# Kernel tuning notes

Measured on AMD Instinct MI355X. Metric: run time of the kernel, lower is better.

Reference implementation:

```python
import jax, jax.numpy as jnp
import numpy as np

N_EMBED = 1024
N_HEADS = 16
HEAD_SIZE = N_EMBED // N_HEADS
B, T = 4, 2048
LN_EPS = 1e-5


def _layer_norm(x, gamma, beta):
    mu = jnp.mean(x, axis=-1, keepdims=True)
    var = jnp.var(x, axis=-1, keepdims=True)
    return (x - mu) * jax.lax.rsqrt(var + LN_EPS) * gamma + beta


def setup_inputs() -> dict:
    key = jax.random.key(0)
    ks = jax.random.split(key, 12)
    s = 1.0 / np.sqrt(N_EMBED)
    sh = 1.0 / np.sqrt(4 * N_EMBED)
    return {
        "x": jax.random.normal(ks[0], (B, T, N_EMBED), jnp.float32),
        "Wk": jax.random.uniform(ks[1], (N_EMBED, N_EMBED), jnp.float32, -s, s),
        "Wq": jax.random.uniform(ks[2], (N_EMBED, N_EMBED), jnp.float32, -s, s),
        "Wv": jax.random.uniform(ks[3], (N_EMBED, N_EMBED), jnp.float32, -s, s),
        "Wproj": jax.random.uniform(ks[4], (N_EMBED, N_EMBED), jnp.float32, -s, s),
        "bproj": jax.random.uniform(ks[5], (N_EMBED,), jnp.float32, -s, s),
        "W1": jax.random.uniform(ks[6], (N_EMBED, 4 * N_EMBED), jnp.float32, -s, s),
        "b1": jax.random.uniform(ks[7], (4 * N_EMBED,), jnp.float32, -s, s),
        "W2": jax.random.uniform(ks[8], (4 * N_EMBED, N_EMBED), jnp.float32, -sh, sh),
        "b2": jax.random.uniform(ks[9], (N_EMBED,), jnp.float32, -sh, sh),
        "g1": jnp.ones((N_EMBED,), jnp.float32),
        "beta1": jnp.zeros((N_EMBED,), jnp.float32),
        "g2": jnp.ones((N_EMBED,), jnp.float32),
        "beta2": jnp.zeros((N_EMBED,), jnp.float32),
    }


def reference(x, Wk, Wq, Wv, Wproj, bproj, W1, b1, W2, b2, g1, beta1, g2, beta2):
    Bt, Tt, C = x.shape
    h = _layer_norm(x, g1, beta1)
    # project and split heads: (B, H, T, D)
    def heads(W):
        return (h @ W).reshape(Bt, Tt, N_HEADS, HEAD_SIZE).transpose(0, 2, 1, 3)
    q, k, v = heads(Wq), heads(Wk), heads(Wv)
    wei = jnp.einsum("bhtd,bhsd->bhts", q, k) / np.sqrt(HEAD_SIZE)
    causal = jnp.tril(jnp.ones((Tt, Tt), bool))
    wei = jnp.where(causal, wei, -jnp.inf)
    wei = jax.nn.softmax(wei, axis=-1)
    out = jnp.einsum("bhts,bhsd->bhtd", wei, v)
    out = out.transpose(0, 2, 1, 3).reshape(Bt, Tt, C)
    x = x + out @ Wproj + bproj
    h2 = _layer_norm(x, g2, beta2)
    ff = jax.nn.relu(h2 @ W1 + b1) @ W2 + b2
    return x + ff
```

## Files before the change

kernel.cpp:

```cpp
#include <hip/hip_runtime.h>
#include <stdint.h>

typedef __bf16 bf16x8 __attribute__((ext_vector_type(8)));
typedef float f32x4 __attribute__((ext_vector_type(4)));
typedef unsigned short u16x8 __attribute__((ext_vector_type(8)));
typedef unsigned short u16x4 __attribute__((ext_vector_type(4)));
typedef unsigned int u32x2 __attribute__((ext_vector_type(2)));
typedef float fvec4 __attribute__((ext_vector_type(4)));

__device__ __forceinline__ unsigned short f2b(float f) {
  unsigned u = __builtin_bit_cast(unsigned, f);
  return (unsigned short)((u + 0x7fffu + ((u >> 16) & 1u)) >> 16);
}

__device__ __forceinline__ bf16x8 ldfrag(const unsigned short* p) {
  return __builtin_bit_cast(bf16x8, *(const u16x8*)p);
}

__device__ __forceinline__ float fexp2(float x) {
  float r;
  asm("v_exp_f32 %0, %1" : "=v"(r) : "v"(x));
  return r;
}

__device__ __forceinline__ unsigned cvtpk(float a, float b) {
  unsigned r;
  asm("v_cvt_pk_bf16_f32 %0, %1, %2" : "=v"(r) : "v"(a), "v"(b));
  return r;
}

__device__ __forceinline__ void gload_lds16(const void* g, void* l) {
  auto gp = reinterpret_cast<const __attribute__((address_space(1))) void*>(
      reinterpret_cast<uintptr_t>(g));
  auto lp = reinterpret_cast<__attribute__((address_space(3))) void*>(
      reinterpret_cast<uintptr_t>(l));
  __builtin_amdgcn_global_load_lds(gp, lp, 16, 0, 0);
}

__global__ void transpose_cast(const float* __restrict__ W, unsigned short* __restrict__ Wt,
                               int K, int N) {
  __shared__ float tile[32][33];
  const int n0 = blockIdx.x * 32, k0 = blockIdx.y * 32;
  const int tx = threadIdx.x, ty = threadIdx.y;
#pragma unroll
  for (int j = 0; j < 4; ++j)
    tile[ty + j * 8][tx] = W[(size_t)(k0 + ty + j * 8) * N + n0 + tx];
  __syncthreads();
#pragma unroll
  for (int j = 0; j < 4; ++j)
    Wt[(size_t)(n0 + ty + j * 8) * K + k0 + tx] = f2b(tile[tx][ty + j * 8]);
}

__global__ void ln_kernel(const float* __restrict__ X, const float* __restrict__ g,
                          const float* __restrict__ be, unsigned short* __restrict__ H) {
  const int row = (blockIdx.x * blockDim.x + threadIdx.x) >> 6;
  const int l = threadIdx.x & 63;
  const float* xr = X + (size_t)row * 1024;
  fvec4 v[4];
  float s = 0.f, sq = 0.f;
#pragma unroll
  for (int i = 0; i < 4; ++i) {
    v[i] = *(const fvec4*)(xr + i * 256 + l * 4);
#pragma unroll
    for (int j = 0; j < 4; ++j) { s += v[i][j]; sq += v[i][j] * v[i][j]; }
  }
#pragma unroll
  for (int off = 32; off >= 1; off >>= 1) {
    s += __shfl_xor(s, off);
    sq += __shfl_xor(sq, off);
  }
  const float mean = s * (1.f / 1024.f);
  const float var = sq * (1.f / 1024.f) - mean * mean;
  const float rstd = rsqrtf(var + 1e-5f);
#pragma unroll
  for (int i = 0; i < 4; ++i) {
    const int col = i * 256 + l * 4;
    fvec4 gg = *(const fvec4*)(g + col);
    fvec4 bb = *(const fvec4*)(be + col);
    u16x4 o;
#pragma unroll
    for (int j = 0; j < 4; ++j) o[j] = f2b((v[i][j] - mean) * rstd * gg[j] + bb[j]);
    *(u16x4*)(H + (size_t)row * 1024 + col) = o;
  }
}

template <int BM, int BN, int WM, int WN, int NBUF, int NTH, int EPI>
__global__ __launch_bounds__(NTH, 2) void gemm8p(
    const unsigned short* __restrict__ A, const unsigned short* __restrict__ Bt,
    const float* __restrict__ bias, const float* __restrict__ resid,
    float* __restrict__ Cf, unsigned short* __restrict__ Cb,
    unsigned short* __restrict__ pK, unsigned short* __restrict__ pVT,
    int M, int N, int K, int ntiles) {
  constexpr int BK = 32;
  constexpr int ASZ = BM * BK * 2;
  constexpr int BSZ = BN * BK * 2;
  constexpr int BUFSZ = ASZ + BSZ;
  constexpr int NW = NTH / 64;
  static_assert(WM * WN == NW, "wave grid");
  constexpr int MF = BM / (WM * 16);
  constexpr int NF = BN / (WN * 16);
  constexpr int UA = ASZ / (NTH * 16);
  constexpr int UB = BSZ / (NTH * 16);
  constexpr int UNITS = UA + UB;
  constexpr int VMSTEADY = (NBUF - 2) * UNITS;
  static_assert(UA * NTH * 16 == ASZ && UB * NTH * 16 == BSZ, "unit split");
  __shared__ __align__(16) char lds[NBUF * BUFSZ];

  const int tid = threadIdx.x;
  const int w = tid >> 6, l = tid & 63;
  const int wr = w / WN, wc = w % WN;
  const int kg = l >> 4, fr = l & 15;
  const int xtiles = N / BN;
  const int nblk = (int)gridDim.x;

  int Aoff[MF], Boff[NF];
#pragma unroll
  for (int m = 0; m < MF; ++m) {
    const int r = wr * (MF * 16) + m * 16 + fr;
    Aoff[m] = r * 64 + ((kg * 16) ^ (((r >> 1) & 3) << 4));
  }
#pragma unroll
  for (int n = 0; n < NF; ++n) {
    const int r = wc * (NF * 16) + n * 16 + fr;
    Boff[n] = ASZ + r * 64 + ((kg * 16) ^ (((r >> 1) & 3) << 4));
  }

  for (int tl = (int)blockIdx.x; tl < ntiles; tl += nblk) {
    if (tl != (int)blockIdx.x) __builtin_amdgcn_s_barrier();
    const int q8 = ntiles >> 3;
    const int swz = (tl & 7) * q8 + (tl >> 3);
    const size_t am0 = (size_t)(swz / xtiles) * BM;
    const size_t bn0 = (size_t)(swz % xtiles) * BN;

    const char* src[UNITS];
#pragma unroll
    for (int u = 0; u < UA; ++u) {
      const int flatq = u * NTH + tid;
      const int row = flatq >> 2;
      const int scb = ((flatq & 3) << 4) ^ (((row >> 1) & 3) << 4);
      src[u] = (const char*)(A + (am0 + row) * K) + scb;
    }
#pragma unroll
    for (int u = 0; u < UB; ++u) {
      const int flatq = u * NTH + tid;
      const int row = flatq >> 2;
      const int scb = ((flatq & 3) << 4) ^ (((row >> 1) & 3) << 4);
      src[UA + u] = (const char*)(Bt + (bn0 + row) * K) + scb;
    }

    f32x4 acc[MF][NF];
#pragma unroll
    for (int m = 0; m < MF; ++m)
#pragma unroll
      for (int n = 0; n < NF; ++n) acc[m][n] = (f32x4){0.f, 0.f, 0.f, 0.f};

    auto stage = [&](int sb) {
#pragma unroll
      for (int u = 0; u < UNITS; ++u) {
        gload_lds16(src[u], lds + sb * BUFSZ + u * (NTH * 16) + tid * 16);
        src[u] += 64;
      }
    };

    const int NT = K / BK;
#pragma unroll
    for (int p = 0; p < NBUF - 1; ++p) stage(p);
    asm volatile("s_waitcnt vmcnt(%0)" ::"i"(VMSTEADY) : "memory");
    __builtin_amdgcn_s_barrier();

    int cb0 = 0, sb = NBUF - 1;
    for (int kt = 0; kt < NT; ++kt) {
      if (kt + NBUF - 1 < NT) stage(sb);
      bf16x8 af[MF], bf[NF];
#pragma unroll
      for (int m = 0; m < MF; ++m)
        af[m] = ldfrag((const unsigned short*)(lds + cb0 + Aoff[m]));
#pragma unroll
      for (int n = 0; n < NF; ++n)
        bf[n] = ldfrag((const unsigned short*)(lds + cb0 + Boff[n]));
      __builtin_amdgcn_s_setprio(1);
#pragma unroll
      for (int m = 0; m < MF; ++m)
#pragma unroll
        for (int n = 0; n < NF; ++n)
          acc[m][n] = __builtin_amdgcn_mfma_f32_16x16x32_bf16(af[m], bf[n], acc[m][n], 0, 0, 0);
      __builtin_amdgcn_s_setprio(0);
      if (kt + NBUF - 1 < NT) {
        asm volatile("s_waitcnt vmcnt(%0)" ::"i"(VMSTEADY) : "memory");
        __builtin_amdgcn_s_barrier();
      } else if (kt + 2 < NT) {
        asm volatile("s_waitcnt vmcnt(%0)" ::"i"(UNITS) : "memory");
        __builtin_amdgcn_s_barrier();
      } else if (kt + 1 < NT) {
        asm volatile("s_waitcnt vmcnt(0)" ::: "memory");
        __builtin_amdgcn_s_barrier();
      }
      cb0 += BUFSZ;
      if (cb0 == NBUF * BUFSZ) cb0 = 0;
      sb += 1;
      if (sb == NBUF) sb = 0;
    }

#pragma unroll
    for (int m = 0; m < MF; ++m) {
      const size_t row0 = am0 + wr * (MF * 16) + m * 16 + kg * 4;
#pragma unroll
      for (int n = 0; n < NF; ++n) {
        const size_t col = bn0 + wc * (NF * 16) + n * 16 + fr;
        if (EPI == 3) {
          if (bn0 < 1024) {
#pragma unroll
            for (int r = 0; r < 4; ++r) Cb[(row0 + r) * 1024 + col] = f2b(acc[m][n][r]);
          } else if (bn0 < 2048) {
#pragma unroll
            for (int r = 0; r < 4; ++r) pK[(row0 + r) * 1024 + col - 1024] = f2b(acc[m][n][r]);
          } else {
            const int c2 = (int)col - 2048;
            const int hh = c2 >> 6, dd = c2 & 63;
            const int bb = (int)(row0 >> 11), tt = (int)(row0 & 2047);
            u16x4 pv;
#pragma unroll
            for (int r = 0; r < 4; ++r) pv[r] = f2b(acc[m][n][r]);
            *(u16x4*)(pVT + (((size_t)bb * 16 + hh) * 64 + dd) * 2048 + tt) = pv;
          }
        } else {
          const float bv = (EPI >= 1) ? bias[col] : 0.f;
#pragma unroll
          for (int r = 0; r < 4; ++r) {
            const size_t idx = (row0 + r) * N + col;
            float v = acc[m][n][r] + bv;
            if (EPI == 1) v = fmaxf(v, 0.f);
            if (EPI == 2) {
              Cf[idx] = v + resid[idx];
            } else {
              Cb[idx] = f2b(v);
            }
          }
        }
      }
    }
  }
}

#define PSTR 40
#define SC2 0.18033688f
__global__ __launch_bounds__(256, 3) void attn_kernel(const unsigned short* __restrict__ Qb,
                                                      const unsigned short* __restrict__ Kb,
                                                      const unsigned short* __restrict__ VT,
                                                      unsigned short* __restrict__ ATT) {
  __shared__ unsigned short Pl[4][32 * PSTR];
  const int tid = threadIdx.x;
  const int w = tid >> 6, l = tid & 63;
  const int kg = l >> 4, fr = l & 15;
  const int bh = blockIdx.x;
  const int b = bh >> 4, h = bh & 15;
  const int qt = 15 - (int)blockIdx.y;
  const int q0 = qt * 128 + w * 32;
  const size_t rbase = (size_t)b * 2048;
  const unsigned short* vtb = VT + (size_t)bh * 64 * 2048;

  bf16x8 bq[2][2];
#pragma unroll
  for (int qg = 0; qg < 2; ++qg) {
    const unsigned short* qrow = Qb + (rbase + q0 + qg * 16 + fr) * 1024 + h * 64;
#pragma unroll
    for (int c = 0; c < 2; ++c) bq[qg][c] = ldfrag(qrow + c * 32 + kg * 8);
  }

  f32x4 o[2][4];
#pragma unroll
  for (int qg = 0; qg < 2; ++qg)
#pragma unroll
    for (int nd = 0; nd < 4; ++nd) o[qg][nd] = (f32x4){0.f, 0.f, 0.f, 0.f};
  float m_run2[2] = {-1e30f, -1e30f}, l_run[2] = {0.f, 0.f};

  auto loadK = [&](int s0, bf16x8 (&ka)[2][2]) {
#pragma unroll
    for (int sg = 0; sg < 2; ++sg) {
      const unsigned short* krow = Kb + (rbase + s0 + sg * 16 + fr) * 1024 + h * 64;
      ka[sg][0] = ldfrag(krow + kg * 8);
      ka[sg][1] = ldfrag(krow + 32 + kg * 8);
    }
  };

  auto process = [&](int s0, bf16x8 (&ka)[2][2]) {
    bf16x8 vb[4];
#pragma unroll
    for (int nd = 0; nd < 4; ++nd)
      vb[nd] = ldfrag(vtb + (size_t)(nd * 16 + fr) * 2048 + s0 + kg * 8);

    f32x4 st[2][2];
#pragma unroll
    for (int sg = 0; sg < 2; ++sg)
#pragma unroll
      for (int qg = 0; qg < 2; ++qg) {
        st[sg][qg] = (f32x4){0.f, 0.f, 0.f, 0.f};
        st[sg][qg] = __builtin_amdgcn_mfma_f32_16x16x32_bf16(ka[sg][0], bq[qg][0], st[sg][qg], 0, 0, 0);
        st[sg][qg] = __builtin_amdgcn_mfma_f32_16x16x32_bf16(ka[sg][1], bq[qg][1], st[sg][qg], 0, 0, 0);
      }

#pragma unroll
    for (int qg = 0; qg < 2; ++qg) {
      const int qa = q0 + qg * 16 + fr;
      float vals[8];
      float tmax = -1e30f;
#pragma unroll
      for (int sg = 0; sg < 2; ++sg)
#pragma unroll
        for (int r = 0; r < 4; ++r) {
          const int sa = s0 + sg * 16 + kg * 4 + r;
          float v = (sa > qa) ? -1e30f : st[sg][qg][r];
          vals[sg * 4 + r] = v;
          tmax = fmaxf(tmax, v);
        }
      tmax = fmaxf(tmax, __shfl_xor(tmax, 16));
      tmax = fmaxf(tmax, __shfl_xor(tmax, 32));
      const float tm2 = tmax * SC2;
      if (__any(tm2 > m_run2[qg] + 8.f)) {
        const float m_new2 = fmaxf(m_run2[qg], tm2);
        const float alpha = fexp2(m_run2[qg] - m_new2);
        m_run2[qg] = m_new2;
        l_run[qg] *= alpha;
        float al[4];
#pragma unroll
        for (int r = 0; r < 4; ++r) al[r] = __shfl(alpha, kg * 4 + r);
#pragma unroll
        for (int nd = 0; nd < 4; ++nd)
#pragma unroll
          for (int r = 0; r < 4; ++r) o[qg][nd][r] *= al[r];
      }
      const float nm2 = -m_run2[qg];
      float psum = 0.f;
      unsigned pk[4];
#pragma unroll
      for (int i = 0; i < 4; ++i) {
        const float p0 = fexp2(__builtin_fmaf(vals[2 * i], SC2, nm2));
        const float p1 = fexp2(__builtin_fmaf(vals[2 * i + 1], SC2, nm2));
        psum += p0 + p1;
        pk[i] = cvtpk(p0, p1);
      }
      psum += __shfl_xor(psum, 16);
      psum += __shfl_xor(psum, 32);
      l_run[qg] += psum;
      u32x2 w0 = {pk[0], pk[1]};
      u32x2 w1 = {pk[2], pk[3]};
      *(u32x2*)(&Pl[w][(qg * 16 + fr) * PSTR + kg * 4]) = w0;
      *(u32x2*)(&Pl[w][(qg * 16 + fr) * PSTR + 16 + kg * 4]) = w1;
    }

    bf16x8 pa[2];
#pragma unroll
    for (int qg = 0; qg < 2; ++qg)
      pa[qg] = ldfrag(&Pl[w][(qg * 16 + fr) * PSTR + kg * 8]);
#pragma unroll
    for (int nd = 0; nd < 4; ++nd)
#pragma unroll
      for (int qg = 0; qg < 2; ++qg)
        o[qg][nd] = __builtin_amdgcn_mfma_f32_16x16x32_bf16(pa[qg], vb[nd], o[qg][nd], 0, 0, 0);
  };

  bf16x8 kaA[2][2], kaB[2][2];
  loadK(0, kaA);
  const int nt = (q0 >> 5) + 1;
  for (int t = 0; t < nt; t += 2) {
    if (t + 1 < nt) loadK((t + 1) << 5, kaB);
    process(t << 5, kaA);
    if (t + 1 < nt) {
      if (t + 2 < nt) loadK((t + 2) << 5, kaA);
      process((t + 1) << 5, kaB);
    }
  }

#pragma unroll
  for (int qg = 0; qg < 2; ++qg) {
    const float li = __builtin_amdgcn_rcpf(l_run[qg]);
    float linv[4];
#pragma unroll
    for (int r = 0; r < 4; ++r) linv[r] = __shfl(li, kg * 4 + r);
#pragma unroll
    for (int nd = 0; nd < 4; ++nd)
#pragma unroll
      for (int r = 0; r < 4; ++r) {
        const size_t row = rbase + q0 + qg * 16 + kg * 4 + r;
        ATT[row * 1024 + h * 64 + nd * 16 + fr] = f2b(o[qg][nd][r] * linv[r]);
      }
  }
}

extern "C" void kernel_launch(void* const* d_in, const int* in_sizes, int n_in, void* d_out,
                              int out_size, void* d_ws, size_t ws_size, hipStream_t stream) {
  const float* x = (const float*)d_in[0];
  const float* Wk = (const float*)d_in[1];
  const float* Wq = (const float*)d_in[2];
  const float* Wv = (const float*)d_in[3];
  const float* Wproj = (const float*)d_in[4];
  const float* bproj = (const float*)d_in[5];
  const float* W1 = (const float*)d_in[6];
  const float* b1 = (const float*)d_in[7];
  const float* W2 = (const float*)d_in[8];
  const float* b2 = (const float*)d_in[9];
  const float* g1 = (const float*)d_in[10];
  const float* beta1 = (const float*)d_in[11];
  const float* g2 = (const float*)d_in[12];
  const float* beta2 = (const float*)d_in[13];
  float* out = (float*)d_out;
  unsigned short* wsu = (unsigned short*)d_ws;

  const size_t o_qkvW = 0;
  const size_t o_projW = o_qkvW + 3072 * 1024;
  const size_t o_W1 = o_projW + 1024 * 1024;
  const size_t o_W2 = o_W1 + 4096 * 1024;
  const size_t o_H = o_W2 + 1024 * 4096;
  const size_t o_Q = o_H + (size_t)8192 * 1024;
  const size_t o_K = o_Q + (size_t)8192 * 1024;
  const size_t o_VT = o_K + (size_t)8192 * 1024;
  const size_t o_ATT = o_VT + (size_t)8192 * 1024;
  const size_t o_FF1 = o_Q;

  dim3 tpb(32, 8);
  transpose_cast<<<dim3(32, 32), tpb, 0, stream>>>(Wq, wsu + o_qkvW, 1024, 1024);
  transpose_cast<<<dim3(32, 32), tpb, 0, stream>>>(Wk, wsu + o_qkvW + 1024 * 1024, 1024, 1024);
  transpose_cast<<<dim3(32, 32), tpb, 0, stream>>>(Wv, wsu + o_qkvW + 2 * 1024 * 1024, 1024, 1024);
  transpose_cast<<<dim3(32, 32), tpb, 0, stream>>>(Wproj, wsu + o_projW, 1024, 1024);
  transpose_cast<<<dim3(128, 32), tpb, 0, stream>>>(W1, wsu + o_W1, 1024, 4096);
  transpose_cast<<<dim3(32, 128), tpb, 0, stream>>>(W2, wsu + o_W2, 4096, 1024);

  ln_kernel<<<2048, 256, 0, stream>>>(x, g1, beta1, wsu + o_H);

  gemm8p<256, 128, 2, 2, 3, 256, 3><<<512, 256, 0, stream>>>(
      wsu + o_H, wsu + o_qkvW, nullptr, nullptr, nullptr, wsu + o_Q, wsu + o_K, wsu + o_VT,
      8192, 3072, 1024, 768);

  attn_kernel<<<dim3(64, 16), 256, 0, stream>>>(wsu + o_Q, wsu + o_K, wsu + o_VT, wsu + o_ATT);

  gemm8p<256, 128, 2, 2, 3, 256, 2><<<256, 256, 0, stream>>>(
      wsu + o_ATT, wsu + o_projW, bproj, x, out, nullptr, nullptr, nullptr,
      8192, 1024, 1024, 256);

  ln_kernel<<<2048, 256, 0, stream>>>(out, g2, beta2, wsu + o_H);

  gemm8p<256, 256, 2, 4, 4, 512, 1><<<512, 512, 0, stream>>>(
      wsu + o_H, wsu + o_W1, b1, nullptr, nullptr, wsu + o_FF1, nullptr, nullptr,
      8192, 4096, 1024, 512);

  gemm8p<256, 128, 2, 2, 3, 256, 2><<<256, 256, 0, stream>>>(
      wsu + o_FF1, wsu + o_W2, b2, out, out, nullptr, nullptr, nullptr,
      8192, 1024, 4096, 256);
}
```

Measured before the change: 405.6 us.

## Stage K tiles through swizzled LDS triple buffer with 64-key blocks in attention

```diff
diff --git a/kernel.cpp b/kernel.cpp
--- a/kernel.cpp
+++ b/kernel.cpp
@@ -242,13 +242,14 @@
   }
 }
 
-#define PSTR 40
+#define PSTR 72
 #define SC2 0.18033688f
 __global__ __launch_bounds__(256, 3) void attn_kernel(const unsigned short* __restrict__ Qb,
                                                       const unsigned short* __restrict__ Kb,
                                                       const unsigned short* __restrict__ VT,
                                                       unsigned short* __restrict__ ATT) {
-  __shared__ unsigned short Pl[4][32 * PSTR];
+  __shared__ __align__(16) char ldsK[3 * 8192];
+  __shared__ __align__(16) unsigned short Pl[4][32 * PSTR];
   const int tid = threadIdx.x;
   const int w = tid >> 6, l = tid & 63;
   const int kg = l >> 4, fr = l & 15;
@@ -259,6 +260,17 @@
   const size_t rbase = (size_t)b * 2048;
   const unsigned short* vtb = VT + (size_t)bh * 64 * 2048;
 
+  const int rowoff = tid >> 3;
+  const int cbsw = ((tid & 7) * 16) ^ ((rowoff & 7) << 4);
+  const char* ksrc = (const char*)(Kb + rbase * 1024 + h * 64) + (size_t)rowoff * 2048 + cbsw;
+
+  int koff[4][2];
+#pragma unroll
+  for (int sg = 0; sg < 4; ++sg)
+#pragma unroll
+    for (int c = 0; c < 2; ++c)
+      koff[sg][c] = (sg * 16 + fr) * 128 + ((c * 64 + kg * 16) ^ ((fr & 7) << 4));
+
   bf16x8 bq[2][2];
 #pragma unroll
   for (int qg = 0; qg < 2; ++qg) {
@@ -274,38 +286,40 @@
     for (int nd = 0; nd < 4; ++nd) o[qg][nd] = (f32x4){0.f, 0.f, 0.f, 0.f};
   float m_run2[2] = {-1e30f, -1e30f}, l_run[2] = {0.f, 0.f};
 
-  auto loadK = [&](int s0, bf16x8 (&ka)[2][2]) {
-#pragma unroll
-    for (int sg = 0; sg < 2; ++sg) {
-      const unsigned short* krow = Kb + (rbase + s0 + sg * 16 + fr) * 1024 + h * 64;
-      ka[sg][0] = ldfrag(krow + kg * 8);
-      ka[sg][1] = ldfrag(krow + 32 + kg * 8);
-    }
+  auto stage = [&](int t, int sbuf) {
+    gload_lds16(ksrc + (size_t)(t * 64) * 2048, ldsK + sbuf * 8192 + tid * 16);
+    gload_lds16(ksrc + (size_t)(t * 64 + 32) * 2048, ldsK + sbuf * 8192 + 4096 + tid * 16);
   };
 
-  auto process = [&](int s0, bf16x8 (&ka)[2][2]) {
-    bf16x8 vb[4];
+  auto compute = [&](int s0, int cbb) {
+    if (s0 > q0 + 31) return;
+    bf16x8 vb[4][2];
 #pragma unroll
     for (int nd = 0; nd < 4; ++nd)
-      vb[nd] = ldfrag(vtb + (size_t)(nd * 16 + fr) * 2048 + s0 + kg * 8);
-
-    f32x4 st[2][2];
-#pragma unroll
-    for (int sg = 0; sg < 2; ++sg)
+#pragma unroll
+      for (int ks = 0; ks < 2; ++ks)
+        vb[nd][ks] = ldfrag(vtb + (size_t)(nd * 16 + fr) * 2048 + s0 + ks * 32 + kg * 8);
+
+    f32x4 st[4][2];
+#pragma unroll
+    for (int sg = 0; sg < 4; ++sg) {
+      const bf16x8 ka0 = ldfrag((const unsigned short*)(ldsK + cbb + koff[sg][0]));
+      const bf16x8 ka1 = ldfrag((const unsigned short*)(ldsK + cbb + koff[sg][1]));
 #pragma unroll
       for (int qg = 0; qg < 2; ++qg) {
         st[sg][qg] = (f32x4){0.f, 0.f, 0.f, 0.f};
-        st[sg][qg] = __builtin_amdgcn_mfma_f32_16x16x32_bf16(ka[sg][0], bq[qg][0], st[sg][qg], 0, 0, 0);
-        st[sg][qg] = __builtin_amdgcn_mfma_f32_16x16x32_bf16(ka[sg][1], bq[qg][1], st[sg][qg], 0, 0, 0);
-      }
+        st[sg][qg] = __builtin_amdgcn_mfma_f32_16x16x32_bf16(ka0, bq[qg][0], st[sg][qg], 0, 0, 0);
+        st[sg][qg] = __builtin_amdgcn_mfma_f32_16x16x32_bf16(ka1, bq[qg][1], st[sg][qg], 0, 0, 0);
+      }
+    }
 
 #pragma unroll
     for (int qg = 0; qg < 2; ++qg) {
       const int qa = q0 + qg * 16 + fr;
-      float vals[8];
+      float vals[16];
       float tmax = -1e30f;
 #pragma unroll
-      for (int sg = 0; sg < 2; ++sg)
+      for (int sg = 0; sg < 4; ++sg)
 #pragma unroll
         for (int r = 0; r < 4; ++r) {
           const int sa = s0 + sg * 16 + kg * 4 + r;
@@ -331,9 +345,9 @@
       }
       const float nm2 = -m_run2[qg];
       float psum = 0.f;
-      unsigned pk[4];
-#pragma unroll
-      for (int i = 0; i < 4; ++i) {
+      unsigned pk[8];
+#pragma unroll
+      for (int i = 0; i < 8; ++i) {
         const float p0 = fexp2(__builtin_fmaf(vals[2 * i], SC2, nm2));
         const float p1 = fexp2(__builtin_fmaf(vals[2 * i + 1], SC2, nm2));
         psum += p0 + p1;
@@ -342,33 +356,42 @@
       psum += __shfl_xor(psum, 16);
       psum += __shfl_xor(psum, 32);
       l_run[qg] += psum;
-      u32x2 w0 = {pk[0], pk[1]};
-      u32x2 w1 = {pk[2], pk[3]};
-      *(u32x2*)(&Pl[w][(qg * 16 + fr) * PSTR + kg * 4]) = w0;
-      *(u32x2*)(&Pl[w][(qg * 16 + fr) * PSTR + 16 + kg * 4]) = w1;
-    }
-
-    bf16x8 pa[2];
+#pragma unroll
+      for (int sg = 0; sg < 4; ++sg) {
+        u32x2 w2 = {pk[2 * sg], pk[2 * sg + 1]};
+        *(u32x2*)(&Pl[w][(qg * 16 + fr) * PSTR + sg * 16 + kg * 4]) = w2;
+      }
+    }
+
 #pragma unroll
     for (int qg = 0; qg < 2; ++qg)
-      pa[qg] = ldfrag(&Pl[w][(qg * 16 + fr) * PSTR + kg * 8]);
-#pragma unroll
-    for (int nd = 0; nd < 4; ++nd)
-#pragma unroll
-      for (int qg = 0; qg < 2; ++qg)
-        o[qg][nd] = __builtin_amdgcn_mfma_f32_16x16x32_bf16(pa[qg], vb[nd], o[qg][nd], 0, 0, 0);
+#pragma unroll
+      for (int ks = 0; ks < 2; ++ks) {
+        const bf16x8 pa = ldfrag(&Pl[w][(qg * 16 + fr) * PSTR + ks * 32 + kg * 8]);
+#pragma unroll
+        for (int nd = 0; nd < 4; ++nd)
+          o[qg][nd] = __builtin_amdgcn_mfma_f32_16x16x32_bf16(pa, vb[nd][ks], o[qg][nd], 0, 0, 0);
+      }
   };
 
-  bf16x8 kaA[2][2], kaB[2][2];
-  loadK(0, kaA);
-  const int nt = (q0 >> 5) + 1;
-  for (int t = 0; t < nt; t += 2) {
-    if (t + 1 < nt) loadK((t + 1) << 5, kaB);
-    process(t << 5, kaA);
-    if (t + 1 < nt) {
-      if (t + 2 < nt) loadK((t + 2) << 5, kaA);
-      process((t + 1) << 5, kaB);
-    }
+  const int NT = 2 * qt + 2;
+  stage(0, 0);
+  stage(1, 1);
+  asm volatile("s_waitcnt vmcnt(2)" ::: "memory");
+  __builtin_amdgcn_s_barrier();
+  int cb = 0, sb = 2;
+  for (int t = 0; t < NT; ++t) {
+    if (t + 2 < NT) stage(t + 2, sb);
+    compute(t * 64, cb * 8192);
+    if (t + 2 < NT) {
+      asm volatile("s_waitcnt vmcnt(2)" ::: "memory");
+      __builtin_amdgcn_s_barrier();
+    } else if (t + 1 < NT) {
+      asm volatile("s_waitcnt vmcnt(0)" ::: "memory");
+      __builtin_amdgcn_s_barrier();
+    }
+    cb += 1; if (cb == 3) cb = 0;
+    sb += 1; if (sb == 3) sb = 0;
   }
 
 #pragma unroll
```

Result: faster. 355.4 us (-12.4%).
